# Optimization experiments

Hardware: AMD Instinct MI355X
Metric: run time of the kernel (lower is better)

The kernel has to match this reference:

```python
import jax, jax.numpy as jnp
import numpy as np

WINDOW_SIZE = 11
SIGMA = 1.5
C1 = 0.01 ** 2
C2 = 0.03 ** 2
L1_WEIGHT = 1.0
SSIM_WEIGHT = 1.0


def _gaussian_window(channels, window_size=WINDOW_SIZE, sigma=SIGMA):
    x = np.arange(window_size, dtype=np.float32) - window_size // 2
    g = np.exp(-(x ** 2) / (2.0 * sigma ** 2))
    g = g / g.sum()
    w2d = np.outer(g, g).astype(np.float32)  # [ws, ws]
    # depthwise kernel layout OIHW with I=1, O=channels
    return jnp.asarray(np.tile(w2d[None, None], (channels, 1, 1, 1)))


def _dwconv(x, w):
    pad = WINDOW_SIZE // 2
    return jax.lax.conv_general_dilated(
        x, w, window_strides=(1, 1), padding=[(pad, pad), (pad, pad)],
        dimension_numbers=('NCHW', 'OIHW', 'NCHW'),
        feature_group_count=x.shape[1])


def setup_inputs() -> dict:
    key = jax.random.key(0)
    k1, k2 = jax.random.split(key)
    shape = (16, 3, 512, 512)
    outputs = jax.random.uniform(k1, shape, dtype=jnp.float32)
    labels = jax.random.uniform(k2, shape, dtype=jnp.float32)
    return {"outputs": outputs, "labels": labels}


def reference(outputs, labels):
    img1, img2 = outputs, labels
    channel = img1.shape[1]
    window = _gaussian_window(channel).astype(img1.dtype)

    mu1 = _dwconv(img1, window)
    mu2 = _dwconv(img2, window)
    mu1_sq = mu1 * mu1
    mu2_sq = mu2 * mu2
    mu1_mu2 = mu1 * mu2
    sigma1_sq = _dwconv(img1 * img1, window) - mu1_sq
    sigma2_sq = _dwconv(img2 * img2, window) - mu2_sq
    sigma12 = _dwconv(img1 * img2, window) - mu1_mu2

    ssim_map = ((2 * mu1_mu2 + C1) * (2 * sigma12 + C2)) / (
        (mu1_sq + mu2_sq + C1) * (sigma1_sq + sigma2_sq + C2))
    ssim = jnp.mean(ssim_map)

    l1_loss = jnp.mean(jnp.abs(outputs - labels))
    ssim_loss = 1.0 - ssim
    return L1_WEIGHT * l1_loss + SSIM_WEIGHT * ssim_loss
```

## Files before the change

### kernel.cpp

```cpp
#include <hip/hip_runtime.h>
#include <hip/hip_bf16.h>
#include <math.h>

#define IMG 512
#define TW 64
#define TH 32
#define NTX 8
#define NTY 16
#define NIMG 48
#define NBLOCKS (NTX * NTY * NIMG)
#define NPIX (16LL * 3 * 512 * 512)

#define C1F 0.0001f
#define C2F 0.0009f


typedef __attribute__((ext_vector_type(4))) short short4v;
typedef __attribute__((ext_vector_type(8))) short short8;
typedef __attribute__((ext_vector_type(4))) float float4v;
typedef __attribute__((ext_vector_type(2))) unsigned uint2v;
typedef __attribute__((ext_vector_type(4))) unsigned uint4v;

__device__ __forceinline__ float4v mfma16(short4v a, short4v b, float4v c) {
#if defined(__HIP_DEVICE_COMPILE__)
    return __builtin_amdgcn_mfma_f32_16x16x16bf16_1k(a, b, c, 0, 0, 0);
#else
    return c;
#endif
}

#define GW0 0.00102838f
#define GW1 0.00759877f
#define GW2 0.03600077f
#define GW3 0.10936069f
#define GW4 0.21300539f
#define GW5 0.26601172f

__device__ __forceinline__ unsigned short f2bf(float f) {
    unsigned u = __builtin_bit_cast(unsigned, f);
    u += 0x7FFF + ((u >> 16) & 1);
    return (unsigned short)(u >> 16);
}
__device__ __forceinline__ unsigned pk2(float a, float b) {
    __hip_bfloat162 h = __float22bfloat162_rn(make_float2(a, b));
    unsigned u;
    __builtin_memcpy(&u, &h, 4);
    return u;
}

#define BC4(U) __builtin_bit_cast(short4v, U)

#define HCONV_RG(SROW_EXPR, ROW_EXPR, DSTX, DSTY, DSTS, DSTP)                  \
    {                                                                          \
        const int srow_ = (SROW_EXPR);                                         \
        const int gr_   = r00 + (ROW_EXPR);                                    \
        const bool ok_  = colok && (unsigned)gr_ < 512u;                       \
        float4 xf0 = zf, xf1 = zf, yf0 = zf, yf1 = zf;                         \
        if (ok_) {                                                             \
            const size_t o_ = (size_t)gr_ * IMG + cbase;                       \
            xf0 = *(const float4*)(xi + o_);                                   \
            xf1 = *(const float4*)(xi + o_ + 4);                               \
            yf0 = *(const float4*)(yi + o_);                                   \
            yf1 = *(const float4*)(yi + o_ + 4);                               \
        }                                                                      \
        uint4v ux_ = (uint4v){pk2(xf0.x, xf0.y), pk2(xf0.z, xf0.w),            \
                              pk2(xf1.x, xf1.y), pk2(xf1.z, xf1.w)};           \
        uint4v uy_ = (uint4v){pk2(yf0.x, yf0.y), pk2(yf0.z, yf0.w),            \
                              pk2(yf1.x, yf1.y), pk2(yf1.z, yf1.w)};           \
        uint4v u2_ = (uint4v){                                                 \
            pk2(fmaf(xf0.x,xf0.x,yf0.x*yf0.x), fmaf(xf0.y,xf0.y,yf0.y*yf0.y)), \
            pk2(fmaf(xf0.z,xf0.z,yf0.z*yf0.z), fmaf(xf0.w,xf0.w,yf0.w*yf0.w)), \
            pk2(fmaf(xf1.x,xf1.x,yf1.x*yf1.x), fmaf(xf1.y,xf1.y,yf1.y*yf1.y)), \
            pk2(fmaf(xf1.z,xf1.z,yf1.z*yf1.z), fmaf(xf1.w,xf1.w,yf1.w*yf1.w))};\
        uint4v u3_ = (uint4v){                                                 \
            pk2(xf0.x*yf0.x, xf0.y*yf0.y), pk2(xf0.z*yf0.z, xf0.w*yf0.w),      \
            pk2(xf1.x*yf1.x, xf1.y*yf1.y), pk2(xf1.z*yf1.z, xf1.w*yf1.w)};     \
        float4v d_;                                                            \
        d_ = __builtin_amdgcn_mfma_f32_16x16x32_bf16(                          \
                 __builtin_bit_cast(short8, ux_), bh, zero4, 0, 0, 0);         \
        DSTX = (uint2v){pk2(d_[0], d_[1]), pk2(d_[2], d_[3])};                 \
        d_ = __builtin_amdgcn_mfma_f32_16x16x32_bf16(                          \
                 __builtin_bit_cast(short8, uy_), bh, zero4, 0, 0, 0);         \
        DSTY = (uint2v){pk2(d_[0], d_[1]), pk2(d_[2], d_[3])};                 \
        d_ = __builtin_amdgcn_mfma_f32_16x16x32_bf16(                          \
                 __builtin_bit_cast(short8, u2_), bh, zero4, 0, 0, 0);         \
        DSTS = (uint2v){pk2(d_[0], d_[1]), pk2(d_[2], d_[3])};                 \
        d_ = __builtin_amdgcn_mfma_f32_16x16x32_bf16(                          \
                 __builtin_bit_cast(short8, u3_), bh, zero4, 0, 0, 0);         \
        DSTP = (uint2v){pk2(d_[0], d_[1]), pk2(d_[2], d_[3])};                 \
        if ((unsigned)(q - 1) <= 1u && (unsigned)(srow_ - 5) <= 31u)           \
            l1_loc += fabsf(xf0.x-yf0.x)+fabsf(xf0.y-yf0.y)                    \
                    + fabsf(xf0.z-yf0.z)+fabsf(xf0.w-yf0.w)                    \
                    + fabsf(xf1.x-yf1.x)+fabsf(xf1.y-yf1.y)                    \
                    + fabsf(xf1.z-yf1.z)+fabsf(xf1.w-yf1.w);                   \
    }

#define SSIM_ACC(M1, M2, EE, PP)                                               \
    _Pragma("unroll")                                                          \
    for (int r_ = 0; r_ < 4; ++r_) {                                           \
        float mu1 = (M1)[r_], mu2 = (M2)[r_];                                  \
        float e   = (EE)[r_], e12 = (PP)[r_];                                  \
        float p = mu1 * mu2;                                                   \
        float s = fmaf(mu1, mu1, mu2 * mu2);                                   \
        float num1 = fmaf(2.f, p, C1F);                                        \
        float num2 = fmaf(2.f, e12 - p, C2F);                                  \
        float den1 = s + C1F;                                                  \
        float den2 = (e - s) + C2F;                                            \
        ssim_loc = fmaf(num1 * num2,                                           \
                        __builtin_amdgcn_rcpf(den1 * den2), ssim_loc);         \
    }

__global__ __launch_bounds__(256, 5)
void ssim_tile_kernel(const float* __restrict__ xg, const float* __restrict__ yg,
                      float* __restrict__ partials) {
    __shared__ unsigned short gwtbl[16];
    __shared__ float red[8];

    const int tid  = threadIdx.x;
    const int lane = tid & 63;
    const int w    = tid >> 6;
    const int q    = lane >> 4;
    const int n16  = lane & 15;

    const int img = blockIdx.z;
    const int r00  = blockIdx.y * TH - 5;
    const int c00a = blockIdx.x * TW - 8;
    const float* __restrict__ xi = xg + (size_t)img * (IMG * IMG);
    const float* __restrict__ yi = yg + (size_t)img * (IMG * IMG);

    if (tid < 16) {
        const float gwf[11] = {GW0, GW1, GW2, GW3, GW4, GW5, GW4, GW3, GW2, GW1, GW0};
        unsigned short v = 0;
        #pragma unroll
        for (int t = 0; t < 11; ++t)
            if (tid == t) v = f2bf(gwf[t]);
        gwtbl[tid] = v;
    }
    __syncthreads();

    short8 bh;
    short4v bv0, bv1;
    {
        int baseh = q * 8 - n16 - 3;
        #pragma unroll
        for (int j = 0; j < 8; ++j)
            bh[j] = (short)gwtbl[min((unsigned)(baseh + j), 15u)];
        int base0 = q * 4 - n16, base1 = q * 4 + 16 - n16;
        #pragma unroll
        for (int j = 0; j < 4; ++j) {
            bv0[j] = (short)gwtbl[min((unsigned)(base0 + j), 15u)];
            bv1[j] = (short)gwtbl[min((unsigned)(base1 + j), 15u)];
        }
    }

    const int cbase = c00a + w * 16 + q * 8;
    const bool colok = (unsigned)cbase < 512u;
    const float4v zero4 = {0.f, 0.f, 0.f, 0.f};
    const float4 zf = make_float4(0.f, 0.f, 0.f, 0.f);

    float l1_loc = 0.f;
    uint2v d0x, d0y, d0s, d0p;
    uint2v e1x, e1y, e1s, e1p;
    uint2v f2x, f2y, f2s, f2p;

    HCONV_RG(n16,            n16,                 d0x, d0y, d0s, d0p)
    HCONV_RG(16 + n16,       16 + n16,            e1x, e1y, e1s, e1p)
    HCONV_RG(32 + n16,       min(32 + n16, 41),   f2x, f2y, f2s, f2p)

    float ssim_loc = 0.f;
    {
        float4v am1 = mfma16(BC4(d0x), bv0, mfma16(BC4(e1x), bv1, zero4));
        float4v am2 = mfma16(BC4(d0y), bv0, mfma16(BC4(e1y), bv1, zero4));
        float4v ae  = mfma16(BC4(d0s), bv0, mfma16(BC4(e1s), bv1, zero4));
        float4v ap  = mfma16(BC4(d0p), bv0, mfma16(BC4(e1p), bv1, zero4));
        SSIM_ACC(am1, am2, ae, ap)
    }
    {
        float4v bm1 = mfma16(BC4(e1x), bv0, mfma16(BC4(f2x), bv1, zero4));
        float4v bm2 = mfma16(BC4(e1y), bv0, mfma16(BC4(f2y), bv1, zero4));
        float4v be  = mfma16(BC4(e1s), bv0, mfma16(BC4(f2s), bv1, zero4));
        float4v bp  = mfma16(BC4(e1p), bv0, mfma16(BC4(f2p), bv1, zero4));
        SSIM_ACC(bm1, bm2, be, bp)
    }

    #pragma unroll
    for (int off = 32; off > 0; off >>= 1) {
        ssim_loc += __shfl_down(ssim_loc, off);
        l1_loc   += __shfl_down(l1_loc, off);
    }
    if (lane == 0) {
        red[w] = ssim_loc;
        red[4 + w] = l1_loc;
    }
    __syncthreads();
    if (tid == 0) {
        float ss = red[0] + red[1] + red[2] + red[3];
        float ll = red[4] + red[5] + red[6] + red[7];
        int bid = blockIdx.x + NTX * (blockIdx.y + NTY * blockIdx.z);
        partials[bid] = ss;
        partials[NBLOCKS + bid] = ll;
    }
}

__global__ __launch_bounds__(1024)
void finalize_kernel(const float* __restrict__ partials, float* __restrict__ out) {
    __shared__ double rs[16], rl[16];
    const int tid = threadIdx.x;
    double ss = 0.0, ll = 0.0;
    for (int i = tid; i < NBLOCKS; i += 1024) {
        ss += (double)partials[i];
        ll += (double)partials[NBLOCKS + i];
    }
    #pragma unroll
    for (int off = 32; off > 0; off >>= 1) {
        ss += __shfl_down(ss, off);
        ll += __shfl_down(ll, off);
    }
    int wave = tid >> 6, lane = tid & 63;
    if (lane == 0) { rs[wave] = ss; rl[wave] = ll; }
    __syncthreads();
    if (tid == 0) {
        double sst = 0.0, llt = 0.0;
        #pragma unroll
        for (int w = 0; w < 16; ++w) { sst += rs[w]; llt += rl[w]; }
        double invn = 1.0 / (double)NPIX;
        out[0] = (float)(llt * invn + (1.0 - sst * invn));
    }
}

extern "C" void kernel_launch(void* const* d_in, const int* in_sizes, int n_in,
                              void* d_out, int out_size, void* d_ws, size_t ws_size,
                              hipStream_t stream) {
    const float* x = (const float*)d_in[0];
    const float* y = (const float*)d_in[1];
    float* out = (float*)d_out;
    float* partials = (float*)d_ws;

    dim3 grid(NTX, NTY, NIMG);
    ssim_tile_kernel<<<grid, dim3(256), 0, stream>>>(x, y, partials);
    finalize_kernel<<<1, dim3(1024), 0, stream>>>(partials, out);
}
```

Before: 137.9 us.

## Convert SSIM to persistent double-buffered LDS pipeline over multiple tiles per block

Each block now processes 12 tiles in sequence instead of one tile per block. Global loads for the next tile are issued before the MFMA convolution of the current tile. The bf16-packed inputs and products are staged cooperatively in a double-buffered shared-memory array. The aim is to overlap memory latency with compute, and to stop each wave from loading its own halo through separate loads. In exchange it uses a large LDS footprint, lowers occupancy to 2 blocks per CU, adds a barrier per tile, and launches only 512 blocks, which could underfill the GPU.

After: 146.6 us. 6.3% more time.

```diff
diff --git a/kernel.cpp b/kernel.cpp
--- a/kernel.cpp
+++ b/kernel.cpp
@@ -8,12 +8,15 @@
 #define NTX 8
 #define NTY 16
 #define NIMG 48
-#define NBLOCKS (NTX * NTY * NIMG)
+#define TPB 12
+#define NPBLK 512
 #define NPIX (16LL * 3 * 512 * 512)
 
 #define C1F 0.0001f
 #define C2F 0.0009f
 
+#define SROWS 42
+#define SR 88
 
 typedef __attribute__((ext_vector_type(4))) short short4v;
 typedef __attribute__((ext_vector_type(8))) short short8;
@@ -50,49 +53,50 @@
 
 #define BC4(U) __builtin_bit_cast(short4v, U)
 
-#define HCONV_RG(SROW_EXPR, ROW_EXPR, DSTX, DSTY, DSTS, DSTP)                  \
-    {                                                                          \
-        const int srow_ = (SROW_EXPR);                                         \
-        const int gr_   = r00 + (ROW_EXPR);                                    \
-        const bool ok_  = colok && (unsigned)gr_ < 512u;                       \
-        float4 xf0 = zf, xf1 = zf, yf0 = zf, yf1 = zf;                         \
-        if (ok_) {                                                             \
-            const size_t o_ = (size_t)gr_ * IMG + cbase;                       \
-            xf0 = *(const float4*)(xi + o_);                                   \
-            xf1 = *(const float4*)(xi + o_ + 4);                               \
-            yf0 = *(const float4*)(yi + o_);                                   \
-            yf1 = *(const float4*)(yi + o_ + 4);                               \
+#define TCOORD(TT, R00, C00A, XI, YI)                                          \
+    {                                                                          \
+        const int gid_ = gbase + (TT);                                         \
+        XI = xg + ((size_t)(gid_ >> 7) * (IMG * IMG));                         \
+        YI = yg + ((size_t)(gid_ >> 7) * (IMG * IMG));                         \
+        R00  = ((gid_ >> 3) & 15) * TH - 5;                                    \
+        C00A = (gid_ & 7) * TW - 8;                                            \
+    }
+
+#define STAGE_LOAD(PR, G10, R00, C00A, XI, YI, X0, X1, Y0, Y1)                 \
+    {                                                                          \
+        const int gr_ = (R00) + (PR), gc_ = (C00A) + ((G10) << 3);             \
+        const bool rk_ = (unsigned)gr_ < 512u;                                 \
+        const int o_ = gr_ * IMG + gc_;                                        \
+        if (rk_ && (unsigned)gc_ < 512u) {                                     \
+            X0 = *(const float4*)((XI) + o_);                                  \
+            Y0 = *(const float4*)((YI) + o_);                                  \
         }                                                                      \
-        uint4v ux_ = (uint4v){pk2(xf0.x, xf0.y), pk2(xf0.z, xf0.w),            \
-                              pk2(xf1.x, xf1.y), pk2(xf1.z, xf1.w)};           \
-        uint4v uy_ = (uint4v){pk2(yf0.x, yf0.y), pk2(yf0.z, yf0.w),            \
-                              pk2(yf1.x, yf1.y), pk2(yf1.z, yf1.w)};           \
-        uint4v u2_ = (uint4v){                                                 \
-            pk2(fmaf(xf0.x,xf0.x,yf0.x*yf0.x), fmaf(xf0.y,xf0.y,yf0.y*yf0.y)), \
-            pk2(fmaf(xf0.z,xf0.z,yf0.z*yf0.z), fmaf(xf0.w,xf0.w,yf0.w*yf0.w)), \
-            pk2(fmaf(xf1.x,xf1.x,yf1.x*yf1.x), fmaf(xf1.y,xf1.y,yf1.y*yf1.y)), \
-            pk2(fmaf(xf1.z,xf1.z,yf1.z*yf1.z), fmaf(xf1.w,xf1.w,yf1.w*yf1.w))};\
-        uint4v u3_ = (uint4v){                                                 \
-            pk2(xf0.x*yf0.x, xf0.y*yf0.y), pk2(xf0.z*yf0.z, xf0.w*yf0.w),      \
-            pk2(xf1.x*yf1.x, xf1.y*yf1.y), pk2(xf1.z*yf1.z, xf1.w*yf1.w)};     \
-        float4v d_;                                                            \
-        d_ = __builtin_amdgcn_mfma_f32_16x16x32_bf16(                          \
-                 __builtin_bit_cast(short8, ux_), bh, zero4, 0, 0, 0);         \
-        DSTX = (uint2v){pk2(d_[0], d_[1]), pk2(d_[2], d_[3])};                 \
-        d_ = __builtin_amdgcn_mfma_f32_16x16x32_bf16(                          \
-                 __builtin_bit_cast(short8, uy_), bh, zero4, 0, 0, 0);         \
-        DSTY = (uint2v){pk2(d_[0], d_[1]), pk2(d_[2], d_[3])};                 \
-        d_ = __builtin_amdgcn_mfma_f32_16x16x32_bf16(                          \
-                 __builtin_bit_cast(short8, u2_), bh, zero4, 0, 0, 0);         \
-        DSTS = (uint2v){pk2(d_[0], d_[1]), pk2(d_[2], d_[3])};                 \
-        d_ = __builtin_amdgcn_mfma_f32_16x16x32_bf16(                          \
-                 __builtin_bit_cast(short8, u3_), bh, zero4, 0, 0, 0);         \
-        DSTP = (uint2v){pk2(d_[0], d_[1]), pk2(d_[2], d_[3])};                 \
-        if ((unsigned)(q - 1) <= 1u && (unsigned)(srow_ - 5) <= 31u)           \
-            l1_loc += fabsf(xf0.x-yf0.x)+fabsf(xf0.y-yf0.y)                    \
-                    + fabsf(xf0.z-yf0.z)+fabsf(xf0.w-yf0.w)                    \
-                    + fabsf(xf1.x-yf1.x)+fabsf(xf1.y-yf1.y)                    \
-                    + fabsf(xf1.z-yf1.z)+fabsf(xf1.w-yf1.w);                   \
+        if (rk_ && (unsigned)(gc_ + 4) < 512u) {                               \
+            X1 = *(const float4*)((XI) + o_ + 4);                              \
+            Y1 = *(const float4*)((YI) + o_ + 4);                              \
+        }                                                                      \
+    }
+
+#define STAGE_WRITE(NB, PR, G10, X0, X1, Y0, Y1)                               \
+    {                                                                          \
+        const int pc8_ = (G10) << 3;                                           \
+        *(uint4v*)&sbuf[NB][0][PR][pc8_] = (uint4v){                           \
+            pk2(X0.x, X0.y), pk2(X0.z, X0.w), pk2(X1.x, X1.y), pk2(X1.z, X1.w)};\
+        *(uint4v*)&sbuf[NB][1][PR][pc8_] = (uint4v){                           \
+            pk2(Y0.x, Y0.y), pk2(Y0.z, Y0.w), pk2(Y1.x, Y1.y), pk2(Y1.z, Y1.w)};\
+        *(uint4v*)&sbuf[NB][2][PR][pc8_] = (uint4v){                           \
+            pk2(fmaf(X0.x,X0.x,Y0.x*Y0.x), fmaf(X0.y,X0.y,Y0.y*Y0.y)),         \
+            pk2(fmaf(X0.z,X0.z,Y0.z*Y0.z), fmaf(X0.w,X0.w,Y0.w*Y0.w)),         \
+            pk2(fmaf(X1.x,X1.x,Y1.x*Y1.x), fmaf(X1.y,X1.y,Y1.y*Y1.y)),         \
+            pk2(fmaf(X1.z,X1.z,Y1.z*Y1.z), fmaf(X1.w,X1.w,Y1.w*Y1.w))};        \
+        *(uint4v*)&sbuf[NB][3][PR][pc8_] = (uint4v){                           \
+            pk2(X0.x*Y0.x, X0.y*Y0.y), pk2(X0.z*Y0.z, X0.w*Y0.w),              \
+            pk2(X1.x*Y1.x, X1.y*Y1.y), pk2(X1.z*Y1.z, X1.w*Y1.w)};             \
+        if ((unsigned)((PR) - 5) <= 31u && (unsigned)((G10) - 1) <= 7u)        \
+            l1_loc += fabsf(X0.x-Y0.x)+fabsf(X0.y-Y0.y)                        \
+                    + fabsf(X0.z-Y0.z)+fabsf(X0.w-Y0.w)                        \
+                    + fabsf(X1.x-Y1.x)+fabsf(X1.y-Y1.y)                        \
+                    + fabsf(X1.z-Y1.z)+fabsf(X1.w-Y1.w);                       \
     }
 
 #define SSIM_ACC(M1, M2, EE, PP)                                               \
@@ -110,9 +114,29 @@
                         __builtin_amdgcn_rcpf(den1 * den2), ssim_loc);         \
     }
 
-__global__ __launch_bounds__(256, 5)
-void ssim_tile_kernel(const float* __restrict__ xg, const float* __restrict__ yg,
+#define HCONV(ROWE, DX, DY, DS, DP)                                            \
+    {                                                                          \
+        const int row_ = (ROWE);                                               \
+        const int co_ = w * 16 + q * 8;                                        \
+        short8 a_; float4v d_;                                                 \
+        a_ = *(const short8*)&sbuf[cur][0][row_][co_];                         \
+        d_ = __builtin_amdgcn_mfma_f32_16x16x32_bf16(a_, bh, zero4, 0, 0, 0);  \
+        DX = (uint2v){pk2(d_[0], d_[1]), pk2(d_[2], d_[3])};                   \
+        a_ = *(const short8*)&sbuf[cur][1][row_][co_];                         \
+        d_ = __builtin_amdgcn_mfma_f32_16x16x32_bf16(a_, bh, zero4, 0, 0, 0);  \
+        DY = (uint2v){pk2(d_[0], d_[1]), pk2(d_[2], d_[3])};                   \
+        a_ = *(const short8*)&sbuf[cur][2][row_][co_];                         \
+        d_ = __builtin_amdgcn_mfma_f32_16x16x32_bf16(a_, bh, zero4, 0, 0, 0);  \
+        DS = (uint2v){pk2(d_[0], d_[1]), pk2(d_[2], d_[3])};                   \
+        a_ = *(const short8*)&sbuf[cur][3][row_][co_];                         \
+        d_ = __builtin_amdgcn_mfma_f32_16x16x32_bf16(a_, bh, zero4, 0, 0, 0);  \
+        DP = (uint2v){pk2(d_[0], d_[1]), pk2(d_[2], d_[3])};                   \
+    }
+
+__global__ __launch_bounds__(256, 2)
+void ssim_pipe_kernel(const float* __restrict__ xg, const float* __restrict__ yg,
                       float* __restrict__ partials) {
+    __shared__ unsigned short sbuf[2][4][SROWS][SR];
     __shared__ unsigned short gwtbl[16];
     __shared__ float red[8];
 
@@ -121,12 +145,6 @@
     const int w    = tid >> 6;
     const int q    = lane >> 4;
     const int n16  = lane & 15;
-
-    const int img = blockIdx.z;
-    const int r00  = blockIdx.y * TH - 5;
-    const int c00a = blockIdx.x * TW - 8;
-    const float* __restrict__ xi = xg + (size_t)img * (IMG * IMG);
-    const float* __restrict__ yi = yg + (size_t)img * (IMG * IMG);
 
     if (tid < 16) {
         const float gwf[11] = {GW0, GW1, GW2, GW3, GW4, GW5, GW4, GW3, GW2, GW1, GW0};
@@ -153,34 +171,69 @@
         }
     }
 
-    const int cbase = c00a + w * 16 + q * 8;
-    const bool colok = (unsigned)cbase < 512u;
+    const int pr0 = tid / 10, g0 = tid - pr0 * 10;
+    const int u1x = tid + 256;
+    const int pr1 = u1x / 10, g1 = u1x - pr1 * 10;
+    const bool has1 = (tid < 420 - 256);
+
+    float l1_loc = 0.f, ssim_loc = 0.f;
+    const int gbase = blockIdx.x * TPB;
+    const float4 zf = make_float4(0.f, 0.f, 0.f, 0.f);
     const float4v zero4 = {0.f, 0.f, 0.f, 0.f};
-    const float4 zf = make_float4(0.f, 0.f, 0.f, 0.f);
-
-    float l1_loc = 0.f;
-    uint2v d0x, d0y, d0s, d0p;
-    uint2v e1x, e1y, e1s, e1p;
-    uint2v f2x, f2y, f2s, f2p;
-
-    HCONV_RG(n16,            n16,                 d0x, d0y, d0s, d0p)
-    HCONV_RG(16 + n16,       16 + n16,            e1x, e1y, e1s, e1p)
-    HCONV_RG(32 + n16,       min(32 + n16, 41),   f2x, f2y, f2s, f2p)
-
-    float ssim_loc = 0.f;
+
     {
-        float4v am1 = mfma16(BC4(d0x), bv0, mfma16(BC4(e1x), bv1, zero4));
-        float4v am2 = mfma16(BC4(d0y), bv0, mfma16(BC4(e1y), bv1, zero4));
-        float4v ae  = mfma16(BC4(d0s), bv0, mfma16(BC4(e1s), bv1, zero4));
-        float4v ap  = mfma16(BC4(d0p), bv0, mfma16(BC4(e1p), bv1, zero4));
-        SSIM_ACC(am1, am2, ae, ap)
-    }
-    {
-        float4v bm1 = mfma16(BC4(e1x), bv0, mfma16(BC4(f2x), bv1, zero4));
-        float4v bm2 = mfma16(BC4(e1y), bv0, mfma16(BC4(f2y), bv1, zero4));
-        float4v be  = mfma16(BC4(e1s), bv0, mfma16(BC4(f2s), bv1, zero4));
-        float4v bp  = mfma16(BC4(e1p), bv0, mfma16(BC4(f2p), bv1, zero4));
-        SSIM_ACC(bm1, bm2, be, bp)
+        const float *xi, *yi; int r00, c00a;
+        TCOORD(0, r00, c00a, xi, yi)
+        float4 X00=zf, X01=zf, Y00=zf, Y01=zf, X10=zf, X11=zf, Y10=zf, Y11=zf;
+        STAGE_LOAD(pr0, g0, r00, c00a, xi, yi, X00, X01, Y00, Y01)
+        if (has1) STAGE_LOAD(pr1, g1, r00, c00a, xi, yi, X10, X11, Y10, Y11)
+        STAGE_WRITE(0, pr0, g0, X00, X01, Y00, Y01)
+        if (has1) STAGE_WRITE(0, pr1, g1, X10, X11, Y10, Y11)
+    }
+    __syncthreads();
+
+    int cur = 0;
+    for (int t = 0; t < TPB; ++t) {
+        const bool hn = (t + 1 < TPB);
+
+        float4 X00=zf, X01=zf, Y00=zf, Y01=zf, X10=zf, X11=zf, Y10=zf, Y11=zf;
+        if (hn) {
+            const float *nxi, *nyi; int nr00, nc00a;
+            TCOORD(t + 1, nr00, nc00a, nxi, nyi)
+            STAGE_LOAD(pr0, g0, nr00, nc00a, nxi, nyi, X00, X01, Y00, Y01)
+            if (has1) STAGE_LOAD(pr1, g1, nr00, nc00a, nxi, nyi, X10, X11, Y10, Y11)
+        }
+
+        {
+            uint2v d0x, d0y, d0s, d0p;
+            uint2v e1x, e1y, e1s, e1p;
+            uint2v f2x, f2y, f2s, f2p;
+            HCONV(n16,               d0x, d0y, d0s, d0p)
+            HCONV(16 + n16,          e1x, e1y, e1s, e1p)
+            HCONV(min(32 + n16, 41), f2x, f2y, f2s, f2p)
+
+            {
+                float4v am1 = mfma16(BC4(d0x), bv0, mfma16(BC4(e1x), bv1, zero4));
+                float4v am2 = mfma16(BC4(d0y), bv0, mfma16(BC4(e1y), bv1, zero4));
+                float4v ae  = mfma16(BC4(d0s), bv0, mfma16(BC4(e1s), bv1, zero4));
+                float4v ap  = mfma16(BC4(d0p), bv0, mfma16(BC4(e1p), bv1, zero4));
+                SSIM_ACC(am1, am2, ae, ap)
+            }
+            {
+                float4v bm1 = mfma16(BC4(e1x), bv0, mfma16(BC4(f2x), bv1, zero4));
+                float4v bm2 = mfma16(BC4(e1y), bv0, mfma16(BC4(f2y), bv1, zero4));
+                float4v be  = mfma16(BC4(e1s), bv0, mfma16(BC4(f2s), bv1, zero4));
+                float4v bp  = mfma16(BC4(e1p), bv0, mfma16(BC4(f2p), bv1, zero4));
+                SSIM_ACC(bm1, bm2, be, bp)
+            }
+        }
+
+        if (hn) {
+            STAGE_WRITE(cur ^ 1, pr0, g0, X00, X01, Y00, Y01)
+            if (has1) STAGE_WRITE(cur ^ 1, pr1, g1, X10, X11, Y10, Y11)
+        }
+        __syncthreads();
+        cur ^= 1;
     }
 
     #pragma unroll
@@ -196,20 +249,19 @@
     if (tid == 0) {
         float ss = red[0] + red[1] + red[2] + red[3];
         float ll = red[4] + red[5] + red[6] + red[7];
-        int bid = blockIdx.x + NTX * (blockIdx.y + NTY * blockIdx.z);
-        partials[bid] = ss;
-        partials[NBLOCKS + bid] = ll;
-    }
-}
-
-__global__ __launch_bounds__(1024)
+        partials[blockIdx.x] = ss;
+        partials[NPBLK + blockIdx.x] = ll;
+    }
+}
+
+__global__ __launch_bounds__(256)
 void finalize_kernel(const float* __restrict__ partials, float* __restrict__ out) {
-    __shared__ double rs[16], rl[16];
+    __shared__ double rs[4], rl[4];
     const int tid = threadIdx.x;
     double ss = 0.0, ll = 0.0;
-    for (int i = tid; i < NBLOCKS; i += 1024) {
+    for (int i = tid; i < NPBLK; i += 256) {
         ss += (double)partials[i];
-        ll += (double)partials[NBLOCKS + i];
+        ll += (double)partials[NPBLK + i];
     }
     #pragma unroll
     for (int off = 32; off > 0; off >>= 1) {
@@ -220,9 +272,8 @@
     if (lane == 0) { rs[wave] = ss; rl[wave] = ll; }
     __syncthreads();
     if (tid == 0) {
-        double sst = 0.0, llt = 0.0;
-        #pragma unroll
-        for (int w = 0; w < 16; ++w) { sst += rs[w]; llt += rl[w]; }
+        double sst = rs[0] + rs[1] + rs[2] + rs[3];
+        double llt = rl[0] + rl[1] + rl[2] + rl[3];
         double invn = 1.0 / (double)NPIX;
         out[0] = (float)(llt * invn + (1.0 - sst * invn));
     }
@@ -236,7 +287,6 @@
     float* out = (float*)d_out;
     float* partials = (float*)d_ws;
 
-    dim3 grid(NTX, NTY, NIMG);
-    ssim_tile_kernel<<<grid, dim3(256), 0, stream>>>(x, y, partials);
-    finalize_kernel<<<1, dim3(1024), 0, stream>>>(partials, out);
-}
+    ssim_pipe_kernel<<<dim3(NPBLK), dim3(256), 0, stream>>>(x, y, partials);
+    finalize_kernel<<<1, dim3(256), 0, stream>>>(partials, out);
+}
```

## Stage input tiles in LDS via direct global-to-LDS loads

Applied to the files above, without the earlier changes.

Replaces per-thread global float4 loads in the horizontal convolution with a block-wide cooperative copy of the 42x84 input halo tiles into shared memory using global_load_lds, then reads rows from LDS. Border tiles get explicit zero-fill for out-of-range elements. This aims for more coalesced, asynchronous global traffic and fewer redundant loads across waves. In exchange it uses about 28 KB of LDS per block, which may limit occupancy under the 5-block launch bound, and it adds a sync plus the zero-fill pass.

Measured after the change: 129.5 us. 1.06x faster.

```diff
diff --git a/kernel.cpp b/kernel.cpp
--- a/kernel.cpp
+++ b/kernel.cpp
@@ -15,6 +15,12 @@
 #define C2F 0.0009f
 
 
+#define SR 84
+#define SROWS 42
+#define CHUNKF 256
+#define NCHUNK 14
+#define BUFFLOATS (NCHUNK * CHUNKF)
+
 typedef __attribute__((ext_vector_type(4))) short short4v;
 typedef __attribute__((ext_vector_type(8))) short short8;
 typedef __attribute__((ext_vector_type(4))) float float4v;
@@ -29,6 +35,16 @@
 #endif
 }
 
+__device__ __forceinline__ void gl_lds16(const float* g, float* l) {
+#if defined(__HIP_DEVICE_COMPILE__)
+    __builtin_amdgcn_global_load_lds(
+        (const __attribute__((address_space(1))) void*)g,
+        (__attribute__((address_space(3))) void*)l, 16, 0, 0);
+#else
+    (void)g; (void)l;
+#endif
+}
+
 #define GW0 0.00102838f
 #define GW1 0.00759877f
 #define GW2 0.03600077f
@@ -50,49 +66,44 @@
 
 #define BC4(U) __builtin_bit_cast(short4v, U)
 
-#define HCONV_RG(SROW_EXPR, ROW_EXPR, DSTX, DSTY, DSTS, DSTP)                  \
+#define HCONV_F32(ROWE, SROWE, DX, DY, DS, DP)                                 \
     {                                                                          \
-        const int srow_ = (SROW_EXPR);                                         \
-        const int gr_   = r00 + (ROW_EXPR);                                    \
-        const bool ok_  = colok && (unsigned)gr_ < 512u;                       \
-        float4 xf0 = zf, xf1 = zf, yf0 = zf, yf1 = zf;                         \
-        if (ok_) {                                                             \
-            const size_t o_ = (size_t)gr_ * IMG + cbase;                       \
-            xf0 = *(const float4*)(xi + o_);                                   \
-            xf1 = *(const float4*)(xi + o_ + 4);                               \
-            yf0 = *(const float4*)(yi + o_);                                   \
-            yf1 = *(const float4*)(yi + o_ + 4);                               \
-        }                                                                      \
-        uint4v ux_ = (uint4v){pk2(xf0.x, xf0.y), pk2(xf0.z, xf0.w),            \
-                              pk2(xf1.x, xf1.y), pk2(xf1.z, xf1.w)};           \
-        uint4v uy_ = (uint4v){pk2(yf0.x, yf0.y), pk2(yf0.z, yf0.w),            \
-                              pk2(yf1.x, yf1.y), pk2(yf1.z, yf1.w)};           \
+        const int srow_ = (SROWE);                                             \
+        const int b_ = (ROWE) * SR + co;                                       \
+        float4v x0 = *(const float4v*)&xb[b_];                                 \
+        float4v x1 = *(const float4v*)&xb[b_ + 4];                             \
+        float4v y0 = *(const float4v*)&yb[b_];                                 \
+        float4v y1 = *(const float4v*)&yb[b_ + 4];                             \
+        uint4v ux_ = (uint4v){pk2(x0[0], x0[1]), pk2(x0[2], x0[3]),            \
+                              pk2(x1[0], x1[1]), pk2(x1[2], x1[3])};           \
+        uint4v uy_ = (uint4v){pk2(y0[0], y0[1]), pk2(y0[2], y0[3]),            \
+                              pk2(y1[0], y1[1]), pk2(y1[2], y1[3])};           \
         uint4v u2_ = (uint4v){                                                 \
-            pk2(fmaf(xf0.x,xf0.x,yf0.x*yf0.x), fmaf(xf0.y,xf0.y,yf0.y*yf0.y)), \
-            pk2(fmaf(xf0.z,xf0.z,yf0.z*yf0.z), fmaf(xf0.w,xf0.w,yf0.w*yf0.w)), \
-            pk2(fmaf(xf1.x,xf1.x,yf1.x*yf1.x), fmaf(xf1.y,xf1.y,yf1.y*yf1.y)), \
-            pk2(fmaf(xf1.z,xf1.z,yf1.z*yf1.z), fmaf(xf1.w,xf1.w,yf1.w*yf1.w))};\
+            pk2(fmaf(x0[0],x0[0],y0[0]*y0[0]), fmaf(x0[1],x0[1],y0[1]*y0[1])), \
+            pk2(fmaf(x0[2],x0[2],y0[2]*y0[2]), fmaf(x0[3],x0[3],y0[3]*y0[3])), \
+            pk2(fmaf(x1[0],x1[0],y1[0]*y1[0]), fmaf(x1[1],x1[1],y1[1]*y1[1])), \
+            pk2(fmaf(x1[2],x1[2],y1[2]*y1[2]), fmaf(x1[3],x1[3],y1[3]*y1[3]))};\
         uint4v u3_ = (uint4v){                                                 \
-            pk2(xf0.x*yf0.x, xf0.y*yf0.y), pk2(xf0.z*yf0.z, xf0.w*yf0.w),      \
-            pk2(xf1.x*yf1.x, xf1.y*yf1.y), pk2(xf1.z*yf1.z, xf1.w*yf1.w)};     \
+            pk2(x0[0]*y0[0], x0[1]*y0[1]), pk2(x0[2]*y0[2], x0[3]*y0[3]),      \
+            pk2(x1[0]*y1[0], x1[1]*y1[1]), pk2(x1[2]*y1[2], x1[3]*y1[3])};     \
         float4v d_;                                                            \
         d_ = __builtin_amdgcn_mfma_f32_16x16x32_bf16(                          \
                  __builtin_bit_cast(short8, ux_), bh, zero4, 0, 0, 0);         \
-        DSTX = (uint2v){pk2(d_[0], d_[1]), pk2(d_[2], d_[3])};                 \
+        DX = (uint2v){pk2(d_[0], d_[1]), pk2(d_[2], d_[3])};                   \
         d_ = __builtin_amdgcn_mfma_f32_16x16x32_bf16(                          \
                  __builtin_bit_cast(short8, uy_), bh, zero4, 0, 0, 0);         \
-        DSTY = (uint2v){pk2(d_[0], d_[1]), pk2(d_[2], d_[3])};                 \
+        DY = (uint2v){pk2(d_[0], d_[1]), pk2(d_[2], d_[3])};                   \
         d_ = __builtin_amdgcn_mfma_f32_16x16x32_bf16(                          \
                  __builtin_bit_cast(short8, u2_), bh, zero4, 0, 0, 0);         \
-        DSTS = (uint2v){pk2(d_[0], d_[1]), pk2(d_[2], d_[3])};                 \
+        DS = (uint2v){pk2(d_[0], d_[1]), pk2(d_[2], d_[3])};                   \
         d_ = __builtin_amdgcn_mfma_f32_16x16x32_bf16(                          \
                  __builtin_bit_cast(short8, u3_), bh, zero4, 0, 0, 0);         \
-        DSTP = (uint2v){pk2(d_[0], d_[1]), pk2(d_[2], d_[3])};                 \
+        DP = (uint2v){pk2(d_[0], d_[1]), pk2(d_[2], d_[3])};                   \
         if ((unsigned)(q - 1) <= 1u && (unsigned)(srow_ - 5) <= 31u)           \
-            l1_loc += fabsf(xf0.x-yf0.x)+fabsf(xf0.y-yf0.y)                    \
-                    + fabsf(xf0.z-yf0.z)+fabsf(xf0.w-yf0.w)                    \
-                    + fabsf(xf1.x-yf1.x)+fabsf(xf1.y-yf1.y)                    \
-                    + fabsf(xf1.z-yf1.z)+fabsf(xf1.w-yf1.w);                   \
+            l1_loc += fabsf(x0[0]-y0[0])+fabsf(x0[1]-y0[1])                    \
+                    + fabsf(x0[2]-y0[2])+fabsf(x0[3]-y0[3])                    \
+                    + fabsf(x1[0]-y1[0])+fabsf(x1[1]-y1[1])                    \
+                    + fabsf(x1[2]-y1[2])+fabsf(x1[3]-y1[3]);                   \
     }
 
 #define SSIM_ACC(M1, M2, EE, PP)                                               \
@@ -113,6 +124,8 @@
 __global__ __launch_bounds__(256, 5)
 void ssim_tile_kernel(const float* __restrict__ xg, const float* __restrict__ yg,
                       float* __restrict__ partials) {
+    __shared__ float xb[BUFFLOATS];
+    __shared__ float yb[BUFFLOATS];
     __shared__ unsigned short gwtbl[16];
     __shared__ float red[8];
 
@@ -136,6 +149,37 @@
             if (tid == t) v = f2bf(gwf[t]);
         gwtbl[tid] = v;
     }
+
+    #pragma unroll
+    for (int k = 0; k < 7; ++k) {
+        const int ck = w * 7 + k;
+        const bool isx = (ck < NCHUNK);
+        const int c = isx ? ck : ck - NCHUNK;
+        const int o = c * CHUNKF + lane * 4;
+        const int row = o / SR;
+        const int col = o - row * SR;
+        const int gr = r00 + row, gc = c00a + col;
+        if (((unsigned)gr < 512u) & ((unsigned)gc < 512u)) {
+            const float* src = (isx ? xi : yi) + (size_t)gr * IMG + gc;
+            float* dstb = (isx ? xb : yb) + c * CHUNKF;
+            gl_lds16(src, dstb);
+        }
+    }
+
+    const bool interior = ((unsigned)(blockIdx.x - 1) <= 5u) &
+                          ((unsigned)(blockIdx.y - 1) <= 13u);
+    if (!interior) {
+        const float4v z4 = {0.f, 0.f, 0.f, 0.f};
+        for (int o = tid * 4; o < BUFFLOATS; o += 1024) {
+            int row = o / SR, col = o - row * SR;
+            int gr = r00 + row, gc = c00a + col;
+            if (!(((unsigned)gr < 512u) & ((unsigned)gc < 512u))) {
+                *(float4v*)&xb[o] = z4;
+                *(float4v*)&yb[o] = z4;
+            }
+        }
+    }
+
     __syncthreads();
 
     short8 bh;
@@ -153,19 +197,15 @@
         }
     }
 
-    const int cbase = c00a + w * 16 + q * 8;
-    const bool colok = (unsigned)cbase < 512u;
+    const int co = w * 16 + q * 8;
     const float4v zero4 = {0.f, 0.f, 0.f, 0.f};
-    const float4 zf = make_float4(0.f, 0.f, 0.f, 0.f);
-
     float l1_loc = 0.f;
     uint2v d0x, d0y, d0s, d0p;
     uint2v e1x, e1y, e1s, e1p;
     uint2v f2x, f2y, f2s, f2p;
-
-    HCONV_RG(n16,            n16,                 d0x, d0y, d0s, d0p)
-    HCONV_RG(16 + n16,       16 + n16,            e1x, e1y, e1s, e1p)
-    HCONV_RG(32 + n16,       min(32 + n16, 41),   f2x, f2y, f2s, f2p)
+    HCONV_F32(n16,               n16,      d0x, d0y, d0s, d0p)
+    HCONV_F32(16 + n16,          16 + n16, e1x, e1y, e1s, e1p)
+    HCONV_F32(min(32 + n16, 41), 32 + n16, f2x, f2y, f2s, f2p)
 
     float ssim_loc = 0.f;
     {
```
